# Optimization experiments

Hardware: AMD Instinct MI355X
Metric: run time of the kernel (lower is better)

## Reference

```python
import jax, jax.numpy as jnp
import numpy as np

QB = 127.0  # 2**(8-1) - 1


def ternary_dequant(w):
    # absmean ternary quantization, then dequantize by scale
    scale = jnp.mean(jnp.abs(w))
    w_t = jnp.clip(jnp.round(w / (scale + 1e-8)), -1.0, 1.0)
    w_t = jnp.where(scale == 0.0, jnp.zeros_like(w), w_t)
    return w_t * scale


def activation_quantize(x):
    # per-row (last-dim) absmax int8 fake-quant
    scale = jnp.max(jnp.abs(x), axis=-1, keepdims=True) / QB
    scale = jnp.maximum(scale, 1e-8)
    return jnp.clip(jnp.round(x / scale), -QB, QB) * scale


def setup_inputs() -> dict:
    key = jax.random.key(0)
    kx, kw = jax.random.split(key)
    x = jax.random.normal(kx, (2, 4096, 4096), dtype=jnp.float32)
    # kaiming_uniform-ish init scale; exact init distribution is irrelevant to the math
    bound = 1.0 / np.sqrt(4096)
    weight = jax.random.uniform(kw, (4096, 4096), dtype=jnp.float32,
                                minval=-bound, maxval=bound)
    return {"x": x, "weight": weight}


def reference(x, weight):
    w_q = ternary_dequant(weight)        # [out, in]
    x_q = activation_quantize(x)         # [b, s, in]
    return jnp.einsum('bsi,oi->bso', x_q, w_q)
```

## Files before the change

kernel.cpp:

```cpp
#include <hip/hip_runtime.h>
#include <stdint.h>
#include <stddef.h>


#define K_DIM 4096
#define M_DIM 8192
#define N_DIM 4096

typedef int v4i  __attribute__((ext_vector_type(4)));
typedef int v16i __attribute__((ext_vector_type(16)));

__device__ __forceinline__ void async_copy16(void* lds, const void* g) {
  __builtin_amdgcn_global_load_lds(
      (const __attribute__((address_space(1))) unsigned int*)g,
      (__attribute__((address_space(3))) unsigned int*)lds,
      16, 0, 0);
}

__global__ void k_wsum(const float* __restrict__ w, double* __restrict__ partials) {
  const float4* w4 = (const float4*)w;
  int tid = blockIdx.x * 256 + threadIdx.x;
  double s = 0.0;
  for (int i = tid; i < 4194304; i += 262144) {
    float4 v = w4[i];
    s += (double)fabsf(v.x) + (double)fabsf(v.y) +
         (double)fabsf(v.z) + (double)fabsf(v.w);
  }
  for (int off = 32; off > 0; off >>= 1) s += __shfl_down(s, off);
  __shared__ double lsum[4];
  int lane = threadIdx.x & 63, wid = threadIdx.x >> 6;
  if (lane == 0) lsum[wid] = s;
  __syncthreads();
  if (threadIdx.x == 0)
    partials[blockIdx.x] = lsum[0] + lsum[1] + lsum[2] + lsum[3];
}

__global__ void k_quant(const float* __restrict__ w, const double* __restrict__ partials,
                        float* __restrict__ wscale, char* __restrict__ qw,
                        const float* __restrict__ x, char* __restrict__ qx,
                        float* __restrict__ sx) {
  __shared__ float sT;
  __shared__ float lm[4];
  __shared__ float bscale;

  if (blockIdx.x < 2048) {
    if (threadIdx.x < 64) {
      double s = 0.0;
      for (int i = threadIdx.x; i < 1024; i += 64) s += partials[i];
      for (int off = 32; off > 0; off >>= 1) s += __shfl_down(s, off);
      if (threadIdx.x == 0) {
        float sc = (float)(s / 16777216.0);
        if (blockIdx.x == 0) *wscale = sc;
        float d = sc + 1e-8f;
        unsigned lo = 1u, hi = __float_as_uint(d);
        while (hi - lo > 1u) {
          unsigned mid = lo + ((hi - lo) >> 1);
          if (__uint_as_float(mid) / d > 0.5f) hi = mid; else lo = mid;
        }
        sT = __uint_as_float(hi);
      }
    }
    __syncthreads();
    const float T = sT;
    const float4* w4 = (const float4*)w;
    int* q4 = (int*)qw;
    int tid = blockIdx.x * 256 + threadIdx.x;
    for (int i = tid; i < 4194304; i += 524288) {
      float4 v = w4[i];
      int a = (int)(v.x >= T) - (int)(v.x <= -T);
      int b = (int)(v.y >= T) - (int)(v.y <= -T);
      int c = (int)(v.z >= T) - (int)(v.z <= -T);
      int e = (int)(v.w >= T) - (int)(v.w <= -T);
      q4[i] = (a & 255) | ((b & 255) << 8) | ((c & 255) << 16) | ((e & 255) << 24);
    }
  } else {
    int row = blockIdx.x - 2048;
    const float4* xr = (const float4*)(x + (size_t)row * K_DIM);
    float4 v[4];
    float m = 0.f;
#pragma unroll
    for (int c = 0; c < 4; c++) {
      v[c] = xr[threadIdx.x + c * 256];
      m = fmaxf(m, fmaxf(fmaxf(fabsf(v[c].x), fabsf(v[c].y)),
                         fmaxf(fabsf(v[c].z), fabsf(v[c].w))));
    }
    for (int off = 32; off > 0; off >>= 1) m = fmaxf(m, __shfl_down(m, off));
    int lane = threadIdx.x & 63, wid = threadIdx.x >> 6;
    if (lane == 0) lm[wid] = m;
    __syncthreads();
    if (threadIdx.x == 0) {
      float mm = fmaxf(fmaxf(lm[0], lm[1]), fmaxf(lm[2], lm[3]));
      float sc = fmaxf(mm / 127.0f, 1e-8f);
      bscale = sc;
      sx[row] = sc;
    }
    __syncthreads();
    float sc = bscale;
    int* q4 = (int*)(qx + (size_t)row * K_DIM);
#pragma unroll
    for (int c = 0; c < 4; c++) {
      int a = (int)fmaxf(fminf(rintf(v[c].x / sc), 127.f), -127.f);
      int b = (int)fmaxf(fminf(rintf(v[c].y / sc), 127.f), -127.f);
      int cc = (int)fmaxf(fminf(rintf(v[c].z / sc), 127.f), -127.f);
      int e = (int)fmaxf(fminf(rintf(v[c].w / sc), 127.f), -127.f);
      q4[threadIdx.x + c * 256] = (a & 255) | ((b & 255) << 8) | ((cc & 255) << 16) | ((e & 255) << 24);
    }
  }
}

__global__ __launch_bounds__(512, 2) void k_gemm(const char* __restrict__ qx,
                       const char* __restrict__ qw,
                       const float* __restrict__ sx,
                       const float* __restrict__ wscale,
                       float* __restrict__ out) {
  __shared__ char lds[4][32768];

  const int tid = threadIdx.x;
  const int lane = tid & 63;
  const int wave = tid >> 6;
  const int wr = wave >> 2;
  const int wc = wave & 3;

  const int wg = (blockIdx.x & 7) * 64 + (blockIdx.x >> 3);
  const int bm = wg >> 4;
  const int bn = wg & 15;
  const int rowBase = bm * 256;
  const int colBase = bn * 256;

  const int rl = tid >> 2;
  const int kswz = (((tid & 3) ^ ((rl >> 1) & 3)) << 4);
  const char* gA0 = qx + (size_t)(rowBase + rl) * K_DIM + kswz;
  const char* gA1 = gA0 + (size_t)128 * K_DIM;
  const char* gB0 = qw + (size_t)(colBase + rl) * K_DIM + kswz;
  const char* gB1 = gB0 + (size_t)128 * K_DIM;
  const int dOff = wave << 10;

  const int hi = lane >> 5;
  const int selk = (lane >> 1) & 3;
  const int colk[2] = { ((hi) ^ selk) << 4, ((2 + hi) ^ selk) << 4 };
  const int aBase = ((wr << 7) + (lane & 31)) * 64;
  const int bBase = 16384 + ((wc << 6) + (lane & 31)) * 64;

  v16i acc[4][2] = {};

  auto STAGE = [&](int t) {
    char* b = &lds[t & 3][0];
    const size_t ko = (size_t)t << 6;
    async_copy16(b + dOff,         gA0 + ko);
    async_copy16(b + 8192 + dOff,  gA1 + ko);
    async_copy16(b + 16384 + dOff, gB0 + ko);
    async_copy16(b + 24576 + dOff, gB1 + ko);
  };

  auto BODY = [&](int t, bool doStage) {
    const char* b_ = &lds[t & 3][0];
    v4i bv[2][2], av[4][2];
#pragma unroll
    for (int sn = 0; sn < 2; ++sn)
#pragma unroll
      for (int kk = 0; kk < 2; ++kk)
        bv[sn][kk] = *(const v4i*)(b_ + bBase + sn * 2048 + colk[kk]);
#pragma unroll
    for (int sub = 0; sub < 4; ++sub)
#pragma unroll
      for (int kk = 0; kk < 2; ++kk)
        av[sub][kk] = *(const v4i*)(b_ + aBase + sub * 2048 + colk[kk]);
    if (doStage) STAGE(t + 3);
    asm volatile("" ::: "memory");
    __builtin_amdgcn_s_setprio(1);
#pragma unroll
    for (int kk = 0; kk < 2; ++kk)
#pragma unroll
      for (int sub = 0; sub < 4; ++sub)
#pragma unroll
        for (int sn = 0; sn < 2; ++sn)
          acc[sub][sn] = __builtin_amdgcn_mfma_i32_32x32x32_i8(
              av[sub][kk], bv[sn][kk], acc[sub][sn], 0, 0, 0);
    __builtin_amdgcn_s_setprio(0);
  };

  STAGE(0); STAGE(1); STAGE(2);

  for (int t = 0; t < 61; ++t) {
    asm volatile("s_waitcnt vmcnt(8)" ::: "memory");
    __builtin_amdgcn_s_barrier();
    asm volatile("" ::: "memory");
    BODY(t, true);
  }
  asm volatile("s_waitcnt vmcnt(8)" ::: "memory");
  __builtin_amdgcn_s_barrier();
  asm volatile("" ::: "memory");
  BODY(61, false);
  asm volatile("s_waitcnt vmcnt(4)" ::: "memory");
  __builtin_amdgcn_s_barrier();
  asm volatile("" ::: "memory");
  BODY(62, false);
  asm volatile("s_waitcnt vmcnt(0)" ::: "memory");
  __builtin_amdgcn_s_barrier();
  asm volatile("" ::: "memory");
  BODY(63, false);

  const float swv = *wscale;
  const int colE = colBase + (wc << 6) + (lane & 31);
#pragma unroll
  for (int sub = 0; sub < 4; ++sub) {
#pragma unroll
    for (int reg = 0; reg < 16; ++reg) {
      const int row = rowBase + (wr << 7) + sub * 32 + 4 * hi +
                      (reg & 3) + 8 * (reg >> 2);
      const float s = sx[row] * swv;
#pragma unroll
      for (int sn = 0; sn < 2; ++sn)
        out[(size_t)row * N_DIM + colE + sn * 32] = (float)acc[sub][sn][reg] * s;
    }
  }
}

extern "C" void kernel_launch(void* const* d_in, const int* in_sizes, int n_in,
                              void* d_out, int out_size, void* d_ws, size_t ws_size,
                              hipStream_t stream) {
  const float* x = (const float*)d_in[0];
  const float* w = (const float*)d_in[1];
  float* out = (float*)d_out;
  char* ws = (char*)d_ws;

  double* partials = (double*)ws;
  float* wscale    = (float*)(ws + 8192);
  float* sx        = (float*)(ws + 8448);
  char*  qw        = ws + 41472;
  char*  qx        = ws + 41472 + 16777216;

  k_wsum <<<1024, 256, 0, stream>>>(w, partials);
  k_quant<<<2048 + 8192, 256, 0, stream>>>(w, partials, wscale, qw, x, qx, sx);
  k_gemm <<<32 * 16, 512, 0, stream>>>(qx, qw, sx, wscale, out);
}
```

Measured before the change: 409.7 us.

## Switch GEMM to 16x16x64 int8 MFMA with two-phase staged loads

Replaces the 32x32x32 int8 MFMA tiling with 16x16x64 int8 MFMA, so each wave covers a full 64-wide K step per instruction with an 8x4 grid of 16x16 accumulators. Each K iteration is split into two phases. Each phase loads part of the A fragments from LDS, issues half of the async global-to-LDS copies for the stage three ahead, and runs a block of MFMAs, with extra barriers between phases. The aim is better MFMA throughput and spreading memory traffic across the iteration. The cost is two more barriers per iteration and a new LDS read addressing and swizzle scheme that must match the staging layout.

```diff
diff --git a/kernel.cpp b/kernel.cpp
--- a/kernel.cpp
+++ b/kernel.cpp
@@ -7,8 +7,7 @@
 #define M_DIM 8192
 #define N_DIM 4096
 
-typedef int v4i  __attribute__((ext_vector_type(4)));
-typedef int v16i __attribute__((ext_vector_type(16)));
+typedef int v4i __attribute__((ext_vector_type(4)));
 
 __device__ __forceinline__ void async_copy16(void* lds, const void* g) {
   __builtin_amdgcn_global_load_lds(
@@ -135,13 +134,12 @@
   const char* gB1 = gB0 + (size_t)128 * K_DIM;
   const int dOff = wave << 10;
 
-  const int hi = lane >> 5;
-  const int selk = (lane >> 1) & 3;
-  const int colk[2] = { ((hi) ^ selk) << 4, ((2 + hi) ^ selk) << 4 };
-  const int aBase = ((wr << 7) + (lane & 31)) * 64;
-  const int bBase = 16384 + ((wc << 6) + (lane & 31)) * 64;
-
-  v16i acc[4][2] = {};
+  const int sR = ((lane & 15) >> 1) & 3;
+  const int kro = (((lane >> 4) ^ sR) << 4);
+  const int aOff = ((wr << 7) + (lane & 15)) * 64 + kro;
+  const int bOff = 16384 + ((wc << 6) + (lane & 15)) * 64 + kro;
+
+  v4i acc[8][4] = {};
 
   auto STAGE = [&](int t) {
     char* b = &lds[t & 3][0];
@@ -152,30 +150,48 @@
     async_copy16(b + 24576 + dOff, gB1 + ko);
   };
 
-  auto BODY = [&](int t, bool doStage) {
+  auto PHASES = [&](int t, bool doStage) {
     const char* b_ = &lds[t & 3][0];
-    v4i bv[2][2], av[4][2];
-#pragma unroll
-    for (int sn = 0; sn < 2; ++sn)
-#pragma unroll
-      for (int kk = 0; kk < 2; ++kk)
-        bv[sn][kk] = *(const v4i*)(b_ + bBase + sn * 2048 + colk[kk]);
-#pragma unroll
-    for (int sub = 0; sub < 4; ++sub)
-#pragma unroll
-      for (int kk = 0; kk < 2; ++kk)
-        av[sub][kk] = *(const v4i*)(b_ + aBase + sub * 2048 + colk[kk]);
-    if (doStage) STAGE(t + 3);
-    asm volatile("" ::: "memory");
+    char* sb_ = &lds[(t + 3) & 3][0];
+    const size_t ko_ = (size_t)(t + 3) << 6;
+    v4i bf[4], a0[4];
+#pragma unroll
+    for (int n = 0; n < 4; ++n)
+      bf[n] = *(const v4i*)(b_ + bOff + n * 1024);
+#pragma unroll
+    for (int j = 0; j < 4; ++j)
+      a0[j] = *(const v4i*)(b_ + aOff + j * 1024);
+    if (doStage) {
+      async_copy16(sb_ + dOff,        gA0 + ko_);
+      async_copy16(sb_ + 8192 + dOff, gA1 + ko_);
+    }
+    asm volatile("" ::: "memory");
+    __builtin_amdgcn_s_barrier();
     __builtin_amdgcn_s_setprio(1);
 #pragma unroll
-    for (int kk = 0; kk < 2; ++kk)
-#pragma unroll
-      for (int sub = 0; sub < 4; ++sub)
-#pragma unroll
-        for (int sn = 0; sn < 2; ++sn)
-          acc[sub][sn] = __builtin_amdgcn_mfma_i32_32x32x32_i8(
-              av[sub][kk], bv[sn][kk], acc[sub][sn], 0, 0, 0);
+    for (int m = 0; m < 4; ++m)
+#pragma unroll
+      for (int n = 0; n < 4; ++n)
+        acc[m][n] = __builtin_amdgcn_mfma_i32_16x16x64_i8(a0[m], bf[n], acc[m][n], 0, 0, 0);
+    __builtin_amdgcn_s_setprio(0);
+    asm volatile("" ::: "memory");
+    __builtin_amdgcn_s_barrier();
+    v4i a1[4];
+#pragma unroll
+    for (int j = 0; j < 4; ++j)
+      a1[j] = *(const v4i*)(b_ + aOff + (4 + j) * 1024);
+    if (doStage) {
+      async_copy16(sb_ + 16384 + dOff, gB0 + ko_);
+      async_copy16(sb_ + 24576 + dOff, gB1 + ko_);
+    }
+    asm volatile("" ::: "memory");
+    __builtin_amdgcn_s_barrier();
+    __builtin_amdgcn_s_setprio(1);
+#pragma unroll
+    for (int m = 0; m < 4; ++m)
+#pragma unroll
+      for (int n = 0; n < 4; ++n)
+        acc[4 + m][n] = __builtin_amdgcn_mfma_i32_16x16x64_i8(a1[m], bf[n], acc[4 + m][n], 0, 0, 0);
     __builtin_amdgcn_s_setprio(0);
   };
 
@@ -185,33 +201,33 @@
     asm volatile("s_waitcnt vmcnt(8)" ::: "memory");
     __builtin_amdgcn_s_barrier();
     asm volatile("" ::: "memory");
-    BODY(t, true);
+    PHASES(t, true);
   }
   asm volatile("s_waitcnt vmcnt(8)" ::: "memory");
   __builtin_amdgcn_s_barrier();
   asm volatile("" ::: "memory");
-  BODY(61, false);
+  PHASES(61, false);
   asm volatile("s_waitcnt vmcnt(4)" ::: "memory");
   __builtin_amdgcn_s_barrier();
   asm volatile("" ::: "memory");
-  BODY(62, false);
+  PHASES(62, false);
   asm volatile("s_waitcnt vmcnt(0)" ::: "memory");
   __builtin_amdgcn_s_barrier();
   asm volatile("" ::: "memory");
-  BODY(63, false);
+  PHASES(63, false);
 
   const float swv = *wscale;
-  const int colE = colBase + (wc << 6) + (lane & 31);
-#pragma unroll
-  for (int sub = 0; sub < 4; ++sub) {
-#pragma unroll
-    for (int reg = 0; reg < 16; ++reg) {
-      const int row = rowBase + (wr << 7) + sub * 32 + 4 * hi +
-                      (reg & 3) + 8 * (reg >> 2);
+  const int col0 = colBase + (wc << 6) + (lane & 15);
+  const int row0 = rowBase + (wr << 7) + ((lane >> 4) << 2);
+#pragma unroll
+  for (int m = 0; m < 8; ++m) {
+#pragma unroll
+    for (int r = 0; r < 4; ++r) {
+      const int row = row0 + m * 16 + r;
       const float s = sx[row] * swv;
 #pragma unroll
-      for (int sn = 0; sn < 2; ++sn)
-        out[(size_t)row * N_DIM + colE + sn * 32] = (float)acc[sub][sn][reg] * s;
+      for (int n = 0; n < 4; ++n)
+        out[(size_t)row * N_DIM + col0 + n * 16] = (float)acc[m][n][r] * s;
     }
   }
 }
```

New measurement: 402.4 us. No clear change (-1.8%).

## Shrink GEMM tile to 128x128 with 4 waves and 16x16x64 int8 MFMA

Applied to the files above, without the earlier changes.

The int8 GEMM block tile drops from 256x256 with 8 waves to 128x128 with 4 waves, so the grid grows from 512 to 2048 workgroups. The inner product switches from the 32x32x32 to the 16x16x64 int8 MFMA, with new LDS swizzle offsets and a new epilogue mapping. The aim is more workgroups to fill the CUs and a smaller LDS footprint per block. The cost is lower data reuse per tile, which doubles global and LDS traffic per MAC.

```diff
diff --git a/kernel.cpp b/kernel.cpp
--- a/kernel.cpp
+++ b/kernel.cpp
@@ -7,8 +7,7 @@
 #define M_DIM 8192
 #define N_DIM 4096
 
-typedef int v4i  __attribute__((ext_vector_type(4)));
-typedef int v16i __attribute__((ext_vector_type(16)));
+typedef int v4i __attribute__((ext_vector_type(4)));
 
 __device__ __forceinline__ void async_copy16(void* lds, const void* g) {
   __builtin_amdgcn_global_load_lds(
@@ -108,74 +107,66 @@
   }
 }
 
-__global__ __launch_bounds__(512, 2) void k_gemm(const char* __restrict__ qx,
+__global__ __launch_bounds__(256, 2) void k_gemm(const char* __restrict__ qx,
                        const char* __restrict__ qw,
                        const float* __restrict__ sx,
                        const float* __restrict__ wscale,
                        float* __restrict__ out) {
-  __shared__ char lds[4][32768];
+  __shared__ char lds[4][16384];
 
   const int tid = threadIdx.x;
   const int lane = tid & 63;
   const int wave = tid >> 6;
-  const int wr = wave >> 2;
-  const int wc = wave & 3;
-
-  const int wg = (blockIdx.x & 7) * 64 + (blockIdx.x >> 3);
-  const int bm = wg >> 4;
-  const int bn = wg & 15;
-  const int rowBase = bm * 256;
-  const int colBase = bn * 256;
+  const int wr = wave >> 1;
+  const int wc = wave & 1;
+
+  const int wg = (blockIdx.x & 7) * 256 + (blockIdx.x >> 3);
+  const int bm = wg >> 5;
+  const int bn = wg & 31;
+  const int rowBase = bm * 128;
+  const int colBase = bn * 128;
 
   const int rl = tid >> 2;
   const int kswz = (((tid & 3) ^ ((rl >> 1) & 3)) << 4);
   const char* gA0 = qx + (size_t)(rowBase + rl) * K_DIM + kswz;
-  const char* gA1 = gA0 + (size_t)128 * K_DIM;
+  const char* gA1 = gA0 + (size_t)64 * K_DIM;
   const char* gB0 = qw + (size_t)(colBase + rl) * K_DIM + kswz;
-  const char* gB1 = gB0 + (size_t)128 * K_DIM;
+  const char* gB1 = gB0 + (size_t)64 * K_DIM;
   const int dOff = wave << 10;
 
-  const int hi = lane >> 5;
-  const int selk = (lane >> 1) & 3;
-  const int colk[2] = { ((hi) ^ selk) << 4, ((2 + hi) ^ selk) << 4 };
-  const int aBase = ((wr << 7) + (lane & 31)) * 64;
-  const int bBase = 16384 + ((wc << 6) + (lane & 31)) * 64;
-
-  v16i acc[4][2] = {};
+  const int sR = ((lane & 15) >> 1) & 3;
+  const int kro = (((lane >> 4) ^ sR) << 4);
+  const int aOff = ((wr << 6) + (lane & 15)) * 64 + kro;
+  const int bOff = 8192 + ((wc << 6) + (lane & 15)) * 64 + kro;
+
+  v4i acc[4][4] = {};
 
   auto STAGE = [&](int t) {
     char* b = &lds[t & 3][0];
     const size_t ko = (size_t)t << 6;
     async_copy16(b + dOff,         gA0 + ko);
-    async_copy16(b + 8192 + dOff,  gA1 + ko);
-    async_copy16(b + 16384 + dOff, gB0 + ko);
-    async_copy16(b + 24576 + dOff, gB1 + ko);
+    async_copy16(b + 4096 + dOff,  gA1 + ko);
+    async_copy16(b + 8192 + dOff,  gB0 + ko);
+    async_copy16(b + 12288 + dOff, gB1 + ko);
   };
 
   auto BODY = [&](int t, bool doStage) {
     const char* b_ = &lds[t & 3][0];
-    v4i bv[2][2], av[4][2];
-#pragma unroll
-    for (int sn = 0; sn < 2; ++sn)
-#pragma unroll
-      for (int kk = 0; kk < 2; ++kk)
-        bv[sn][kk] = *(const v4i*)(b_ + bBase + sn * 2048 + colk[kk]);
-#pragma unroll
-    for (int sub = 0; sub < 4; ++sub)
-#pragma unroll
-      for (int kk = 0; kk < 2; ++kk)
-        av[sub][kk] = *(const v4i*)(b_ + aBase + sub * 2048 + colk[kk]);
+    v4i bf[4], af[4];
+#pragma unroll
+    for (int n = 0; n < 4; ++n)
+      bf[n] = *(const v4i*)(b_ + bOff + n * 1024);
+#pragma unroll
+    for (int m = 0; m < 4; ++m)
+      af[m] = *(const v4i*)(b_ + aOff + m * 1024);
     if (doStage) STAGE(t + 3);
     asm volatile("" ::: "memory");
     __builtin_amdgcn_s_setprio(1);
 #pragma unroll
-    for (int kk = 0; kk < 2; ++kk)
-#pragma unroll
-      for (int sub = 0; sub < 4; ++sub)
-#pragma unroll
-        for (int sn = 0; sn < 2; ++sn)
-          acc[sub][sn] = __builtin_amdgcn_mfma_i32_32x32x32_i8(
-              av[sub][kk], bv[sn][kk], acc[sub][sn], 0, 0, 0);
+    for (int m = 0; m < 4; ++m)
+#pragma unroll
+      for (int n = 0; n < 4; ++n)
+        acc[m][n] = __builtin_amdgcn_mfma_i32_16x16x64_i8(af[m], bf[n], acc[m][n], 0, 0, 0);
     __builtin_amdgcn_s_setprio(0);
   };
 
@@ -201,17 +192,17 @@
   BODY(63, false);
 
   const float swv = *wscale;
-  const int colE = colBase + (wc << 6) + (lane & 31);
-#pragma unroll
-  for (int sub = 0; sub < 4; ++sub) {
-#pragma unroll
-    for (int reg = 0; reg < 16; ++reg) {
-      const int row = rowBase + (wr << 7) + sub * 32 + 4 * hi +
-                      (reg & 3) + 8 * (reg >> 2);
+  const int col0 = colBase + (wc << 6) + (lane & 15);
+  const int row0 = rowBase + (wr << 6) + ((lane >> 4) << 2);
+#pragma unroll
+  for (int m = 0; m < 4; ++m) {
+#pragma unroll
+    for (int r = 0; r < 4; ++r) {
+      const int row = row0 + m * 16 + r;
       const float s = sx[row] * swv;
 #pragma unroll
-      for (int sn = 0; sn < 2; ++sn)
-        out[(size_t)row * N_DIM + colE + sn * 32] = (float)acc[sub][sn][reg] * s;
+      for (int n = 0; n < 4; ++n)
+        out[(size_t)row * N_DIM + col0 + n * 16] = (float)acc[m][n][r] * s;
     }
   }
 }
@@ -232,5 +223,5 @@
 
   k_wsum <<<1024, 256, 0, stream>>>(w, partials);
   k_quant<<<2048 + 8192, 256, 0, stream>>>(w, partials, wscale, qw, x, qx, sx);
-  k_gemm <<<32 * 16, 512, 0, stream>>>(qx, qw, sx, wscale, out);
-}
+  k_gemm <<<64 * 32, 256, 0, stream>>>(qx, qw, sx, wscale, out);
+}
```

New measurement: 461.5 us. 1.13x slower.
